# Kernel optimization log

Measured on AMD Instinct MI355X. Metric: run time of the kernel, lower is better.

Reference implementation:

```python
import jax, jax.numpy as jnp
import numpy as np

B, S, IN, E, H, NH = 32, 1024, 16, 128, 256, 4
DH = E // NH
EPS = 1e-5


def _ln(x, g, b):
    mu = jnp.mean(x, axis=-1, keepdims=True)
    var = jnp.mean(jnp.square(x - mu), axis=-1, keepdims=True)
    return (x - mu) * jax.lax.rsqrt(var + EPS) * g + b


def setup_inputs() -> dict:
    key = jax.random.key(0)
    ks = iter(jax.random.split(key, 32))
    n = lambda shape, s=0.02: jax.random.normal(next(ks), shape, jnp.float32) * s
    inp = {
        "x": jax.random.normal(next(ks), (B, S, IN), jnp.float32),
        "mask": jax.random.uniform(next(ks), (B, S), jnp.float32),
        "embed_w": n((E, IN)), "embed_b": jnp.zeros((E,), jnp.float32),
        # 3 encoder layers, params stacked on leading layer axis
        "in_proj_w": n((3, 3 * E, E)), "in_proj_b": jnp.zeros((3, 3 * E), jnp.float32),
        "out_w": n((3, E, E)), "out_b": jnp.zeros((3, E), jnp.float32),
        "ln1_g": jnp.ones((3, E), jnp.float32), "ln1_b": jnp.zeros((3, E), jnp.float32),
        "ln2_g": jnp.ones((3, E), jnp.float32), "ln2_b": jnp.zeros((3, E), jnp.float32),
        "ffn_w1": n((3, E, E)), "ffn_b1": jnp.zeros((3, E), jnp.float32),
        "ffn_w2": n((3, E, E)), "ffn_b2": jnp.zeros((3, E), jnp.float32),
        "cls_w1": n((H, E)), "cls_b1": jnp.zeros((H,), jnp.float32),
        "cls_w2": n((H, H)), "cls_b2": jnp.zeros((H,), jnp.float32),
        "cls_w3": n((H, H)), "cls_b3": jnp.zeros((H,), jnp.float32),
        "cls_w4": n((1, H)), "cls_b4": jnp.zeros((1,), jnp.float32),
    }
    return inp


def _encoder_layer(x, ipw, ipb, ow, ob, g1, b1, g2, b2, w1, fb1, w2, fb2):
    # PyTorch TransformerEncoderLayer, norm_first=False (post-norm), relu FFN
    qkv = x @ ipw.T + ipb                      # [B,S,3E]
    q, k, v = jnp.split(qkv, 3, axis=-1)
    q = q.reshape(B, S, NH, DH).transpose(0, 2, 1, 3)
    k = k.reshape(B, S, NH, DH).transpose(0, 2, 1, 3)
    v = v.reshape(B, S, NH, DH).transpose(0, 2, 1, 3)
    scores = jnp.einsum("bhqd,bhkd->bhqk", q, k) / np.sqrt(DH)  # naive O(S^2) math SDPA
    attn = jax.nn.softmax(scores, axis=-1)
    o = jnp.einsum("bhqk,bhkd->bhqd", attn, v)
    o = o.transpose(0, 2, 1, 3).reshape(B, S, E) @ ow.T + ob
    x = _ln(x + o, g1, b1)
    ff = jax.nn.relu(x @ w1.T + fb1) @ w2.T + fb2
    return _ln(x + ff, g2, b2)


def reference(x, mask, embed_w, embed_b, in_proj_w, in_proj_b, out_w, out_b,
              ln1_g, ln1_b, ln2_g, ln2_b, ffn_w1, ffn_b1, ffn_w2, ffn_b2,
              cls_w1, cls_b1, cls_w2, cls_b2, cls_w3, cls_b3, cls_w4, cls_b4):
    h = jax.nn.relu(x @ embed_w.T + embed_b)   # [B,S,E]
    for i in range(3):
        h = _encoder_layer(h, in_proj_w[i], in_proj_b[i], out_w[i], out_b[i],
                           ln1_g[i], ln1_b[i], ln2_g[i], ln2_b[i],
                           ffn_w1[i], ffn_b1[i], ffn_w2[i], ffn_b2[i])
    pooled = jnp.sum(h * mask[:, :, None], axis=1)  # [B,E] masked sum pool
    z = jax.nn.relu(pooled @ cls_w1.T + cls_b1)
    z = jax.nn.relu(z @ cls_w2.T + cls_b2)
    z = jax.nn.relu(z @ cls_w3.T + cls_b3)
    return jax.nn.sigmoid(z @ cls_w4.T + cls_b4)    # [B,1]
```

## Files before the change

### kernel.cpp

```cpp
#include <hip/hip_runtime.h>
#include <hip/hip_bf16.h>
#include <math.h>

#define B 32
#define S 1024
#define IN_DIM 16
#define E 128
#define NH 4
#define DH 32
#define HDIM 256
#define ROWS (B*S)
#define EPS 1e-5f

#define N_IPW (3*384*128)
#define N_SQ  (3*128*128)
#define NCVT ((N_IPW + 3*N_SQ) / 256)

typedef __bf16 bf16x8 __attribute__((ext_vector_type(8)));
typedef __bf16 bf16x4 __attribute__((ext_vector_type(4)));
typedef __bf16 bf16x2 __attribute__((ext_vector_type(2)));
typedef float f32x4 __attribute__((ext_vector_type(4)));

#define MFMA16 __builtin_amdgcn_mfma_f32_16x16x32_bf16

union BF2U { bf16x2 b; unsigned int u; };
__device__ inline unsigned int pk2(float a, float b) {
    BF2U x; x.b[0] = (__bf16)a; x.b[1] = (__bf16)b; return x.u;
}

union U8 { bf16x8 v8; bf16x4 v4[2]; };
__device__ inline void st8(__bf16* p, bf16x8 v) {
    U8 u; u.v8 = v;
    *(bf16x4*)p = u.v4[0];
    *(bf16x4*)(p + 4) = u.v4[1];
}
__device__ inline bf16x8 ld8(const __bf16* p) {
    U8 u;
    u.v4[0] = *(const bf16x4*)p;
    u.v4[1] = *(const bf16x4*)(p + 4);
    return u.v8;
}

__global__ __launch_bounds__(256) void k_embedcvt(
        const float* __restrict__ ipw, const float* __restrict__ ow,
        const float* __restrict__ w1, const float* __restrict__ w2,
        __bf16* __restrict__ wbo,
        const float* __restrict__ x, const float* __restrict__ W,
        const float* __restrict__ bias, __bf16* __restrict__ hb)
{
    int t = threadIdx.x;
    if (blockIdx.x < NCVT) {
        int i = blockIdx.x * 256 + t;
        float v;
        if (i < N_IPW) v = ipw[i];
        else if (i < N_IPW + N_SQ) v = ow[i - N_IPW];
        else if (i < N_IPW + 2 * N_SQ) v = w1[i - N_IPW - N_SQ];
        else v = w2[i - N_IPW - 2 * N_SQ];
        wbo[i] = (__bf16)v;
        return;
    }
    int row0 = (blockIdx.x - NCVT) * 16;
    __shared__ float xs[16][16];
    xs[t >> 4][t & 15] = x[(row0 + (t >> 4)) * IN_DIM + (t & 15)];
    __syncthreads();
    int sub = t >> 7, tc = t & 127;
    float w[16];
#pragma unroll
    for (int i = 0; i < 16; ++i) w[i] = W[tc * 16 + i];
    float bb = bias[tc];
#pragma unroll
    for (int rr = 0; rr < 8; ++rr) {
        int lr = sub * 8 + rr;
        float acc = bb;
#pragma unroll
        for (int i = 0; i < 16; ++i) acc += xs[lr][i] * w[i];
        hb[(size_t)(row0 + lr) * E + tc] = (__bf16)fmaxf(acc, 0.f);
    }
}

__global__ __launch_bounds__(1024, 4) void k_qkvattn(
        const __bf16* __restrict__ hb, const __bf16* __restrict__ Wip,
        const float* __restrict__ bip, __bf16* __restrict__ O)
{
    __shared__ __attribute__((aligned(16))) __bf16 Ksh[1024][36];
    __shared__ __attribute__((aligned(16))) __bf16 Vsh[32][1036];
    __shared__ __attribute__((aligned(16))) __bf16 Pm[16][16][36];

    int t = threadIdx.x, lane = t & 63, wv = t >> 6;
    int l15 = lane & 15, quad = lane >> 4;
    int lb = ((blockIdx.x & 7) << 5) | (blockIdx.x >> 3);
    int half = lb & 1, bh = lb >> 1;
    int hh = bh & 3, b = bh >> 2;

    const __bf16* hpanel = hb + (size_t)b * S * E;

    const float qscale = 0.1767766952966369f * 1.4426950408889634f * 8388608.0f;
    const float C2 = 1065101558.0f;
    const f32x4 cinit = {C2, C2, C2, C2};
    const f32x4 z4 = {0.f, 0.f, 0.f, 0.f};

    int qrow0 = half * 512 + wv * 32;
    bf16x8 bQ[2];
    {
        bf16x8 bWq[2][4];
#pragma unroll
        for (int df = 0; df < 2; ++df)
#pragma unroll
            for (int kc = 0; kc < 4; ++kc)
                bWq[df][kc] = *(const bf16x8*)&Wip[(size_t)(hh*32 + df*16 + l15)*128 + kc*32 + quad*8];
        float bq0 = bip[hh*32 + l15], bq1 = bip[hh*32 + 16 + l15];
#pragma unroll
        for (int qf = 0; qf < 2; ++qf) {
            bf16x8 af[4];
#pragma unroll
            for (int kc = 0; kc < 4; ++kc)
                af[kc] = *(const bf16x8*)&hpanel[(size_t)(qrow0 + qf*16 + l15)*128 + kc*32 + quad*8];
            f32x4 a0 = z4, a1 = z4;
#pragma unroll
            for (int kc = 0; kc < 4; ++kc) {
                a0 = MFMA16(af[kc], bWq[0][kc], a0, 0, 0, 0);
                a1 = MFMA16(af[kc], bWq[1][kc], a1, 0, 0, 0);
            }
#pragma unroll
            for (int r = 0; r < 4; ++r) {
                Pm[wv][quad*4 + r][l15]      = (__bf16)((a0[r] + bq0) * qscale);
                Pm[wv][quad*4 + r][16 + l15] = (__bf16)((a1[r] + bq1) * qscale);
            }
            __asm__ __volatile__("" ::: "memory");
            bQ[qf] = ld8(&Pm[wv][l15][quad*8]);
            __asm__ __volatile__("" ::: "memory");
        }
    }

    {
        bf16x8 bWk[2][4], bWv[2][4];
#pragma unroll
        for (int df = 0; df < 2; ++df)
#pragma unroll
            for (int kc = 0; kc < 4; ++kc) {
                bWk[df][kc] = *(const bf16x8*)&Wip[(size_t)(128 + hh*32 + df*16 + l15)*128 + kc*32 + quad*8];
                bWv[df][kc] = *(const bf16x8*)&Wip[(size_t)(256 + hh*32 + df*16 + l15)*128 + kc*32 + quad*8];
            }
        float bk0 = bip[128 + hh*32 + l15],  bk1 = bip[128 + hh*32 + 16 + l15];
        float bvb0 = bip[256 + hh*32 + l15], bvb1 = bip[256 + hh*32 + 16 + l15];
#pragma unroll
        for (int c = 0; c < 4; ++c) {
            int srow = c*256 + wv*16 + l15;
            bf16x8 af[4];
#pragma unroll
            for (int kc = 0; kc < 4; ++kc)
                af[kc] = *(const bf16x8*)&hpanel[(size_t)srow*128 + kc*32 + quad*8];
            f32x4 k0 = z4, k1 = z4, v0 = z4, v1 = z4;
#pragma unroll
            for (int kc = 0; kc < 4; ++kc) {
                k0 = MFMA16(af[kc], bWk[0][kc], k0, 0, 0, 0);
                k1 = MFMA16(af[kc], bWk[1][kc], k1, 0, 0, 0);
                v0 = MFMA16(af[kc], bWv[0][kc], v0, 0, 0, 0);
                v1 = MFMA16(af[kc], bWv[1][kc], v1, 0, 0, 0);
            }
            int s0 = c*256 + wv*16 + quad*4;
#pragma unroll
            for (int r = 0; r < 4; ++r) {
                Ksh[s0 + r][l15]      = (__bf16)(k0[r] + bk0);
                Ksh[s0 + r][16 + l15] = (__bf16)(k1[r] + bk1);
            }
            uint2 u0, u1;
            u0.x = pk2(v0[0] + bvb0, v0[1] + bvb0);
            u0.y = pk2(v0[2] + bvb0, v0[3] + bvb0);
            u1.x = pk2(v1[0] + bvb1, v1[1] + bvb1);
            u1.y = pk2(v1[2] + bvb1, v1[3] + bvb1);
            *(uint2*)&Vsh[l15][s0] = u0;
            *(uint2*)&Vsh[16 + l15][s0] = u1;
        }
    }
    __syncthreads();

    bf16x8 vones;
#pragma unroll
    for (int j = 0; j < 8; ++j) vones[j] = (__bf16)1.0f;
    f32x4 o[2][2], ol[2];
#pragma unroll
    for (int qf = 0; qf < 2; ++qf) {
        ol[qf] = z4; o[qf][0] = z4; o[qf][1] = z4;
    }

    for (int c = 0; c < 16; ++c) {
        bf16x8 aK[4], bV[2][2];
#pragma unroll
        for (int ck = 0; ck < 4; ++ck)
            aK[ck] = ld8(&Ksh[c*64 + ck*16 + l15][quad*8]);
#pragma unroll
        for (int kc = 0; kc < 2; ++kc) {
            bV[kc][0] = ld8(&Vsh[l15][c*64 + kc*32 + quad*8]);
            bV[kc][1] = ld8(&Vsh[16 + l15][c*64 + kc*32 + quad*8]);
        }
#pragma unroll
        for (int qf = 0; qf < 2; ++qf) {
            f32x4 sf[4];
#pragma unroll
            for (int ck = 0; ck < 4; ++ck)
                sf[ck] = MFMA16(aK[ck], bQ[qf], cinit, 0, 0, 0);
            uint2 u[4];
#pragma unroll
            for (int ck = 0; ck < 4; ++ck) {
                int i0 = (int)sf[ck][0];
                int i1 = (int)sf[ck][1];
                int i2 = (int)sf[ck][2];
                int i3 = (int)sf[ck][3];
                u[ck].x = __builtin_amdgcn_perm((unsigned)i1, (unsigned)i0, 0x07060302u);
                u[ck].y = __builtin_amdgcn_perm((unsigned)i3, (unsigned)i2, 0x07060302u);
            }
            *(uint2*)&Pm[wv][l15][quad*4]      = u[0];
            *(uint2*)&Pm[wv][l15][16 + quad*4] = u[1];
            __asm__ __volatile__("" ::: "memory");
            {
                bf16x8 ap = ld8(&Pm[wv][l15][quad*8]);
                o[qf][0] = MFMA16(ap, bV[0][0], o[qf][0], 0, 0, 0);
                o[qf][1] = MFMA16(ap, bV[0][1], o[qf][1], 0, 0, 0);
                ol[qf]   = MFMA16(ap, vones, ol[qf], 0, 0, 0);
            }
            __asm__ __volatile__("" ::: "memory");
            *(uint2*)&Pm[wv][l15][quad*4]      = u[2];
            *(uint2*)&Pm[wv][l15][16 + quad*4] = u[3];
            __asm__ __volatile__("" ::: "memory");
            {
                bf16x8 ap = ld8(&Pm[wv][l15][quad*8]);
                o[qf][0] = MFMA16(ap, bV[1][0], o[qf][0], 0, 0, 0);
                o[qf][1] = MFMA16(ap, bV[1][1], o[qf][1], 0, 0, 0);
                ol[qf]   = MFMA16(ap, vones, ol[qf], 0, 0, 0);
            }
            __asm__ __volatile__("" ::: "memory");
        }
    }

#pragma unroll
    for (int qf = 0; qf < 2; ++qf)
#pragma unroll
        for (int r = 0; r < 4; ++r) {
            float linv = 1.f / ol[qf][r];
            int row = half*512 + wv*32 + qf*16 + quad*4 + r;
            __bf16* op = O + ((size_t)(b * S) + row) * E + hh*32;
            op[l15]      = (__bf16)(o[qf][0][r] * linv);
            op[16 + l15] = (__bf16)(o[qf][1][r] * linv);
        }
}

__global__ __launch_bounds__(512, 4) void k_layer2(const __bf16* __restrict__ t0b,
        const __bf16* __restrict__ Wo, const float* __restrict__ ob,
        const float* __restrict__ g1, const float* __restrict__ bt1,
        const __bf16* __restrict__ W1, const float* __restrict__ b1v,
        const __bf16* __restrict__ W2, const float* __restrict__ b2v,
        const float* __restrict__ g2, const float* __restrict__ bt2,
        __bf16* __restrict__ hb)
{
    __shared__ __attribute__((aligned(16))) __bf16 As[64][132];
    __shared__ __attribute__((aligned(16))) __bf16 Ws[128][132];
    __shared__ float red[2][64][2];
    int t = threadIdx.x;
    int m0 = blockIdx.x * 64;
    int arow = t >> 3, acol = (t & 7) * 16;
    int wrow = t >> 2, wcol = (t & 3) * 32;
    {
        const __bf16* Ap = t0b + (size_t)(m0 + arow) * 128 + acol;
#pragma unroll
        for (int j = 0; j < 2; ++j)
            st8(&As[arow][acol + j * 8], *(const bf16x8*)&Ap[j * 8]);
        const __bf16* Wp = Wo + (size_t)wrow * 128 + wcol;
#pragma unroll
        for (int j = 0; j < 4; ++j)
            st8(&Ws[wrow][wcol + j * 8], *(const bf16x8*)&Wp[j * 8]);
    }
    __syncthreads();
    int lane = t & 63, wv = t >> 6;
    int l15 = lane & 15, quad = lane >> 4;
    int nh = wv & 1, mh = wv >> 1;
    f32x4 acc[4];

#pragma unroll
    for (int i = 0; i < 4; ++i) acc[i] = (f32x4){0.f, 0.f, 0.f, 0.f};
#pragma unroll
    for (int kc = 0; kc < 4; ++kc) {
        bf16x8 aw[4], ba;
#pragma unroll
        for (int nc = 0; nc < 4; ++nc)
            aw[nc] = ld8(&Ws[nh * 64 + nc * 16 + l15][kc * 32 + quad * 8]);
        ba = ld8(&As[mh * 16 + l15][kc * 32 + quad * 8]);
#pragma unroll
        for (int nc = 0; nc < 4; ++nc)
            acc[nc] = MFMA16(aw[nc], ba, acc[nc], 0, 0, 0);
    }
    float s1 = 0.f, s2 = 0.f;
    int m = m0 + mh * 16 + l15;
#pragma unroll
    for (int nc = 0; nc < 4; ++nc) {
        float4 bv = *(const float4*)&ob[nh * 64 + nc * 16 + quad * 4];
        bf16x4 rv = *(const bf16x4*)&hb[(size_t)m * 128 + nh * 64 + nc * 16 + quad * 4];
        acc[nc][0] += bv.x + (float)rv[0];
        acc[nc][1] += bv.y + (float)rv[1];
        acc[nc][2] += bv.z + (float)rv[2];
        acc[nc][3] += bv.w + (float)rv[3];
#pragma unroll
        for (int i = 0; i < 4; ++i) {
            s1 += acc[nc][i];
            s2 += acc[nc][i] * acc[nc][i];
        }
    }
    s1 += __shfl_xor(s1, 16); s1 += __shfl_xor(s1, 32);
    s2 += __shfl_xor(s2, 16); s2 += __shfl_xor(s2, 32);
    if (quad == 0) {
        red[nh][mh * 16 + l15][0] = s1;
        red[nh][mh * 16 + l15][1] = s2;
    }
    __syncthreads();
    float mu, rs;
    {
        int r = mh * 16 + l15;
        float S1 = red[0][r][0] + red[1][r][0];
        float S2 = red[0][r][1] + red[1][r][1];
        mu = S1 * (1.f / 128.f);
        float var = S2 * (1.f / 128.f) - mu * mu;
        rs = rsqrtf(var + EPS);
    }
    bf16x4 res2[4];
#pragma unroll
    for (int nc = 0; nc < 4; ++nc) {
        float4 gv = *(const float4*)&g1[nh * 64 + nc * 16 + quad * 4];
        float4 bb = *(const float4*)&bt1[nh * 64 + nc * 16 + quad * 4];
        float o0 = (acc[nc][0] - mu) * rs * gv.x + bb.x;
        float o1 = (acc[nc][1] - mu) * rs * gv.y + bb.y;
        float o2 = (acc[nc][2] - mu) * rs * gv.z + bb.z;
        float o3 = (acc[nc][3] - mu) * rs * gv.w + bb.w;
        bf16x4 xb;
        xb[0] = (__bf16)o0; xb[1] = (__bf16)o1;
        xb[2] = (__bf16)o2; xb[3] = (__bf16)o3;
        res2[nc] = xb;
        *(bf16x4*)&As[mh * 16 + l15][nh * 64 + nc * 16 + quad * 4] = xb;
    }
    {
        const __bf16* Wp = W1 + (size_t)wrow * 128 + wcol;
#pragma unroll
        for (int j = 0; j < 4; ++j)
            st8(&Ws[wrow][wcol + j * 8], *(const bf16x8*)&Wp[j * 8]);
    }
    __syncthreads();

#pragma unroll
    for (int i = 0; i < 4; ++i) acc[i] = (f32x4){0.f, 0.f, 0.f, 0.f};
#pragma unroll
    for (int kc = 0; kc < 4; ++kc) {
        bf16x8 aw[4], ba;
#pragma unroll
        for (int nc = 0; nc < 4; ++nc)
            aw[nc] = ld8(&Ws[nh * 64 + nc * 16 + l15][kc * 32 + quad * 8]);
        ba = ld8(&As[mh * 16 + l15][kc * 32 + quad * 8]);
#pragma unroll
        for (int nc = 0; nc < 4; ++nc)
            acc[nc] = MFMA16(aw[nc], ba, acc[nc], 0, 0, 0);
    }
    __syncthreads();
#pragma unroll
    for (int nc = 0; nc < 4; ++nc) {
        float4 bv = *(const float4*)&b1v[nh * 64 + nc * 16 + quad * 4];
        float v0 = fmaxf(acc[nc][0] + bv.x, 0.f);
        float v1 = fmaxf(acc[nc][1] + bv.y, 0.f);
        float v2 = fmaxf(acc[nc][2] + bv.z, 0.f);
        float v3 = fmaxf(acc[nc][3] + bv.w, 0.f);
        uint2 u; u.x = pk2(v0, v1); u.y = pk2(v2, v3);
        *(uint2*)&As[mh * 16 + l15][nh * 64 + nc * 16 + quad * 4] = u;
    }
    {
        const __bf16* Wp = W2 + (size_t)wrow * 128 + wcol;
#pragma unroll
        for (int j = 0; j < 4; ++j)
            st8(&Ws[wrow][wcol + j * 8], *(const bf16x8*)&Wp[j * 8]);
    }
    __syncthreads();

#pragma unroll
    for (int i = 0; i < 4; ++i) acc[i] = (f32x4){0.f, 0.f, 0.f, 0.f};
#pragma unroll
    for (int kc = 0; kc < 4; ++kc) {
        bf16x8 aw[4], ba;
#pragma unroll
        for (int nc = 0; nc < 4; ++nc)
            aw[nc] = ld8(&Ws[nh * 64 + nc * 16 + l15][kc * 32 + quad * 8]);
        ba = ld8(&As[mh * 16 + l15][kc * 32 + quad * 8]);
#pragma unroll
        for (int nc = 0; nc < 4; ++nc)
            acc[nc] = MFMA16(aw[nc], ba, acc[nc], 0, 0, 0);
    }
    s1 = 0.f; s2 = 0.f;
#pragma unroll
    for (int nc = 0; nc < 4; ++nc) {
        float4 bv = *(const float4*)&b2v[nh * 64 + nc * 16 + quad * 4];
        acc[nc][0] += bv.x + (float)res2[nc][0];
        acc[nc][1] += bv.y + (float)res2[nc][1];
        acc[nc][2] += bv.z + (float)res2[nc][2];
        acc[nc][3] += bv.w + (float)res2[nc][3];
#pragma unroll
        for (int i = 0; i < 4; ++i) {
            s1 += acc[nc][i];
            s2 += acc[nc][i] * acc[nc][i];
        }
    }
    s1 += __shfl_xor(s1, 16); s1 += __shfl_xor(s1, 32);
    s2 += __shfl_xor(s2, 16); s2 += __shfl_xor(s2, 32);
    if (quad == 0) {
        red[nh][mh * 16 + l15][0] = s1;
        red[nh][mh * 16 + l15][1] = s2;
    }
    __syncthreads();
    {
        int r = mh * 16 + l15;
        float S1 = red[0][r][0] + red[1][r][0];
        float S2 = red[0][r][1] + red[1][r][1];
        mu = S1 * (1.f / 128.f);
        float var = S2 * (1.f / 128.f) - mu * mu;
        rs = rsqrtf(var + EPS);
    }
#pragma unroll
    for (int nc = 0; nc < 4; ++nc) {
        float4 gv = *(const float4*)&g2[nh * 64 + nc * 16 + quad * 4];
        float4 bb = *(const float4*)&bt2[nh * 64 + nc * 16 + quad * 4];
        float o0 = (acc[nc][0] - mu) * rs * gv.x + bb.x;
        float o1 = (acc[nc][1] - mu) * rs * gv.y + bb.y;
        float o2 = (acc[nc][2] - mu) * rs * gv.z + bb.z;
        float o3 = (acc[nc][3] - mu) * rs * gv.w + bb.w;
        uint2 u; u.x = pk2(o0, o1); u.y = pk2(o2, o3);
        *(uint2*)&hb[(size_t)m * 128 + nh * 64 + nc * 16 + quad * 4] = u;
    }
}

__global__ __launch_bounds__(128) void k_pool1(const __bf16* __restrict__ h,
        const float* __restrict__ mask, float* __restrict__ part)
{
    int bx = blockIdx.x;
    int b = bx >> 3, ch = bx & 7, t = threadIdx.x;
    float acc = 0.f;
    const __bf16* hp = h + (size_t)(b * S + ch * 128) * E + t;
    const float* mp = mask + b * S + ch * 128;
    for (int s = 0; s < 128; ++s) acc += (float)hp[(size_t)s * E] * mp[s];
    part[(size_t)bx * E + t] = acc;
}

__global__ __launch_bounds__(256) void k_head(const float* __restrict__ part,
        const float* __restrict__ cw1, const float* __restrict__ cb1,
        const float* __restrict__ cw2, const float* __restrict__ cb2,
        const float* __restrict__ cw3, const float* __restrict__ cb3,
        const float* __restrict__ cw4, const float* __restrict__ cb4,
        float* __restrict__ out)
{
    int b = blockIdx.x, t = threadIdx.x;
    __shared__ float p[128], za[256], zb[256];
    __shared__ float red4[4];
    if (t < 128) {
        float a = 0.f;
#pragma unroll
        for (int c = 0; c < 8; ++c) a += part[(size_t)(b * 8 + c) * 128 + t];
        p[t] = a;
    }
    __syncthreads();
    float a1 = cb1[t];
    for (int k = 0; k < 128; ++k) a1 += p[k] * cw1[t * 128 + k];
    za[t] = fmaxf(a1, 0.f);
    __syncthreads();
    float a2 = cb2[t];
    for (int k = 0; k < 256; ++k) a2 += za[k] * cw2[t * 256 + k];
    zb[t] = fmaxf(a2, 0.f);
    __syncthreads();
    float a3 = cb3[t];
    for (int k = 0; k < 256; ++k) a3 += zb[k] * cw3[t * 256 + k];
    float z3 = fmaxf(a3, 0.f);
    float prt = z3 * cw4[t];
#pragma unroll
    for (int o2 = 32; o2; o2 >>= 1) prt += __shfl_xor(prt, o2);
    if ((t & 63) == 0) red4[t >> 6] = prt;
    __syncthreads();
    if (t == 0) {
        float sum = red4[0] + red4[1] + red4[2] + red4[3] + cb4[0];
        out[b] = 1.f / (1.f + __expf(-sum));
    }
}

extern "C" void kernel_launch(void* const* d_in, const int* in_sizes, int n_in,
                              void* d_out, int out_size, void* d_ws, size_t ws_size,
                              hipStream_t stream)
{
    const float* x     = (const float*)d_in[0];
    const float* mask  = (const float*)d_in[1];
    const float* emb_w = (const float*)d_in[2];
    const float* emb_b = (const float*)d_in[3];
    const float* ipw   = (const float*)d_in[4];
    const float* ipb   = (const float*)d_in[5];
    const float* ow    = (const float*)d_in[6];
    const float* ob    = (const float*)d_in[7];
    const float* ln1g  = (const float*)d_in[8];
    const float* ln1b  = (const float*)d_in[9];
    const float* ln2g  = (const float*)d_in[10];
    const float* ln2b  = (const float*)d_in[11];
    const float* w1    = (const float*)d_in[12];
    const float* fb1   = (const float*)d_in[13];
    const float* w2    = (const float*)d_in[14];
    const float* fb2   = (const float*)d_in[15];
    const float* cw1   = (const float*)d_in[16];
    const float* cb1   = (const float*)d_in[17];
    const float* cw2   = (const float*)d_in[18];
    const float* cb2   = (const float*)d_in[19];
    const float* cw3   = (const float*)d_in[20];
    const float* cb3   = (const float*)d_in[21];
    const float* cw4   = (const float*)d_in[22];
    const float* cb4   = (const float*)d_in[23];

    char* p = (char*)d_ws;
    __bf16* hb   = (__bf16*)p;   p += (size_t)ROWS * E * 2;
    p += (size_t)ROWS * 256 * 2;
    p += (size_t)ROWS * 32 * 4 * 2 / 4;
    __bf16* t0b  = (__bf16*)p;   p += (size_t)ROWS * E * 2;
    __bf16* wb   = (__bf16*)p;   p += (size_t)(N_IPW + 3 * N_SQ) * 2;
    float* part  = (float*)p;    p += (size_t)B * 8 * E * 4;

    __bf16* wb_ipw = wb;
    __bf16* wb_ow  = wb + N_IPW;
    __bf16* wb_w1  = wb_ow + N_SQ;
    __bf16* wb_w2  = wb_w1 + N_SQ;

    k_embedcvt<<<NCVT + ROWS / 16, 256, 0, stream>>>(
        ipw, ow, w1, w2, wb, x, emb_w, emb_b, hb);
    for (int L = 0; L < 3; ++L) {
        k_qkvattn<<<B * NH * 2, 1024, 0, stream>>>(
            hb, wb_ipw + (size_t)L * 384 * 128, ipb + L * 384, t0b);
        k_layer2<<<ROWS / 64, 512, 0, stream>>>(
            t0b, wb_ow + (size_t)L * 128 * 128, ob + L * 128,
            ln1g + L * E, ln1b + L * E,
            wb_w1 + (size_t)L * 128 * 128, fb1 + L * 128,
            wb_w2 + (size_t)L * 128 * 128, fb2 + L * 128,
            ln2g + L * E, ln2b + L * E, hb);
    }
    k_pool1<<<B * 8, 128, 0, stream>>>(hb, mask, part);
    k_head<<<B, 256, 0, stream>>>(part, cw1, cb1, cw2, cb2, cw3, cb3, cw4, cb4,
                                  (float*)d_out);
}
```

Before: 316.5 us.

## Switch attention kernel to 32x32 MFMA tiles with register-resident probabilities

Rewrites the attention inner loop to use 32x32x16 bf16 MFMA instead of 16x16x32, with each wave owning 64 query rows. The S tile's accumulator layout is packed straight into the A operand for the PV MFMA, so the LDS round-trip through Pm is no longer needed. The block drops to 512 threads, and the K/V projection loop gains software prefetch of the next h tile. The larger tiles are meant to cut LDS traffic and MFMA issue count, at the cost of more registers per wave and fewer waves per block.

Measured after the change: 291.7 us. 7.8% less time.

```diff
diff --git a/kernel.cpp b/kernel.cpp
--- a/kernel.cpp
+++ b/kernel.cpp
@@ -20,15 +20,17 @@
 typedef __bf16 bf16x4 __attribute__((ext_vector_type(4)));
 typedef __bf16 bf16x2 __attribute__((ext_vector_type(2)));
 typedef float f32x4 __attribute__((ext_vector_type(4)));
+typedef float f32x16 __attribute__((ext_vector_type(16)));
 
 #define MFMA16 __builtin_amdgcn_mfma_f32_16x16x32_bf16
+#define MFMA32 __builtin_amdgcn_mfma_f32_32x32x16_bf16
 
 union BF2U { bf16x2 b; unsigned int u; };
 __device__ inline unsigned int pk2(float a, float b) {
     BF2U x; x.b[0] = (__bf16)a; x.b[1] = (__bf16)b; return x.u;
 }
 
-union U8 { bf16x8 v8; bf16x4 v4[2]; };
+union U8 { bf16x8 v8; bf16x4 v4[2]; unsigned u4[4]; };
 __device__ inline void st8(__bf16* p, bf16x8 v) {
     U8 u; u.v8 = v;
     *(bf16x4*)p = u.v4[0];
@@ -78,16 +80,17 @@
     }
 }
 
-__global__ __launch_bounds__(1024, 4) void k_qkvattn(
+__global__ __launch_bounds__(512, 2) void k_qkvattn(
         const __bf16* __restrict__ hb, const __bf16* __restrict__ Wip,
         const float* __restrict__ bip, __bf16* __restrict__ O)
 {
     __shared__ __attribute__((aligned(16))) __bf16 Ksh[1024][36];
     __shared__ __attribute__((aligned(16))) __bf16 Vsh[32][1036];
-    __shared__ __attribute__((aligned(16))) __bf16 Pm[16][16][36];
+    __shared__ __attribute__((aligned(16))) __bf16 Pm[8][32][36];
 
     int t = threadIdx.x, lane = t & 63, wv = t >> 6;
     int l15 = lane & 15, quad = lane >> 4;
+    int l31 = lane & 31, hi = lane >> 5;
     int lb = ((blockIdx.x & 7) << 5) | (blockIdx.x >> 3);
     int half = lb & 1, bh = lb >> 1;
     int hh = bh & 3, b = bh >> 2;
@@ -96,38 +99,34 @@
 
     const float qscale = 0.1767766952966369f * 1.4426950408889634f * 8388608.0f;
     const float C2 = 1065101558.0f;
-    const f32x4 cinit = {C2, C2, C2, C2};
-    const f32x4 z4 = {0.f, 0.f, 0.f, 0.f};
-
-    int qrow0 = half * 512 + wv * 32;
-    bf16x8 bQ[2];
-    {
-        bf16x8 bWq[2][4];
-#pragma unroll
-        for (int df = 0; df < 2; ++df)
-#pragma unroll
-            for (int kc = 0; kc < 4; ++kc)
-                bWq[df][kc] = *(const bf16x8*)&Wip[(size_t)(hh*32 + df*16 + l15)*128 + kc*32 + quad*8];
-        float bq0 = bip[hh*32 + l15], bq1 = bip[hh*32 + 16 + l15];
-#pragma unroll
-        for (int qf = 0; qf < 2; ++qf) {
-            bf16x8 af[4];
-#pragma unroll
-            for (int kc = 0; kc < 4; ++kc)
-                af[kc] = *(const bf16x8*)&hpanel[(size_t)(qrow0 + qf*16 + l15)*128 + kc*32 + quad*8];
-            f32x4 a0 = z4, a1 = z4;
-#pragma unroll
-            for (int kc = 0; kc < 4; ++kc) {
-                a0 = MFMA16(af[kc], bWq[0][kc], a0, 0, 0, 0);
-                a1 = MFMA16(af[kc], bWq[1][kc], a1, 0, 0, 0);
-            }
-#pragma unroll
-            for (int r = 0; r < 4; ++r) {
-                Pm[wv][quad*4 + r][l15]      = (__bf16)((a0[r] + bq0) * qscale);
-                Pm[wv][quad*4 + r][16 + l15] = (__bf16)((a1[r] + bq1) * qscale);
+    f32x16 cinit16, z16;
+#pragma unroll
+    for (int i = 0; i < 16; ++i) { cinit16[i] = C2; z16[i] = 0.f; }
+
+    bf16x8 bQ[2][2];
+    {
+        bf16x8 bWq[8];
+#pragma unroll
+        for (int ch = 0; ch < 8; ++ch)
+            bWq[ch] = *(const bf16x8*)&Wip[(size_t)(hh*32 + l31)*128 + ch*16 + hi*8];
+        float bq = bip[hh*32 + l31];
+#pragma unroll
+        for (int qt = 0; qt < 2; ++qt) {
+            int qrow0 = half*512 + wv*64 + qt*32;
+            f32x16 aq = z16;
+#pragma unroll
+            for (int ch = 0; ch < 8; ++ch) {
+                bf16x8 ah = *(const bf16x8*)&hpanel[(size_t)(qrow0 + l31)*128 + ch*16 + hi*8];
+                aq = MFMA32(ah, bWq[ch], aq, 0, 0, 0);
+            }
+#pragma unroll
+            for (int r = 0; r < 16; ++r) {
+                int q = (r & 3) + 8*(r >> 2) + 4*hi;
+                Pm[wv][q][l31] = (__bf16)((aq[r] + bq) * qscale);
             }
             __asm__ __volatile__("" ::: "memory");
-            bQ[qf] = ld8(&Pm[wv][l15][quad*8]);
+            bQ[qt][0] = ld8(&Pm[wv][l31][hi*8]);
+            bQ[qt][1] = ld8(&Pm[wv][l31][16 + hi*8]);
             __asm__ __volatile__("" ::: "memory");
         }
     }
@@ -143,13 +142,18 @@
             }
         float bk0 = bip[128 + hh*32 + l15],  bk1 = bip[128 + hh*32 + 16 + l15];
         float bvb0 = bip[256 + hh*32 + l15], bvb1 = bip[256 + hh*32 + 16 + l15];
-#pragma unroll
-        for (int c = 0; c < 4; ++c) {
-            int srow = c*256 + wv*16 + l15;
-            bf16x8 af[4];
-#pragma unroll
-            for (int kc = 0; kc < 4; ++kc)
-                af[kc] = *(const bf16x8*)&hpanel[(size_t)srow*128 + kc*32 + quad*8];
+        int srow = wv*16 + l15;
+        bf16x8 af[4], ag[4];
+#pragma unroll
+        for (int kc = 0; kc < 4; ++kc)
+            af[kc] = *(const bf16x8*)&hpanel[(size_t)srow*128 + kc*32 + quad*8];
+        const f32x4 z4 = {0.f, 0.f, 0.f, 0.f};
+        for (int c = 0; c < 8; ++c) {
+            if (c < 7) {
+#pragma unroll
+                for (int kc = 0; kc < 4; ++kc)
+                    ag[kc] = *(const bf16x8*)&hpanel[(size_t)((c+1)*128 + srow)*128 + kc*32 + quad*8];
+            }
             f32x4 k0 = z4, k1 = z4, v0 = z4, v1 = z4;
 #pragma unroll
             for (int kc = 0; kc < 4; ++kc) {
@@ -158,7 +162,7 @@
                 v0 = MFMA16(af[kc], bWv[0][kc], v0, 0, 0, 0);
                 v1 = MFMA16(af[kc], bWv[1][kc], v1, 0, 0, 0);
             }
-            int s0 = c*256 + wv*16 + quad*4;
+            int s0 = c*128 + wv*16 + quad*4;
 #pragma unroll
             for (int r = 0; r < 4; ++r) {
                 Ksh[s0 + r][l15]      = (__bf16)(k0[r] + bk0);
@@ -171,6 +175,8 @@
             u1.y = pk2(v1[2] + bvb1, v1[3] + bvb1);
             *(uint2*)&Vsh[l15][s0] = u0;
             *(uint2*)&Vsh[16 + l15][s0] = u1;
+#pragma unroll
+            for (int kc = 0; kc < 4; ++kc) af[kc] = ag[kc];
         }
     }
     __syncthreads();
@@ -178,70 +184,58 @@
     bf16x8 vones;
 #pragma unroll
     for (int j = 0; j < 8; ++j) vones[j] = (__bf16)1.0f;
-    f32x4 o[2][2], ol[2];
-#pragma unroll
-    for (int qf = 0; qf < 2; ++qf) {
-        ol[qf] = z4; o[qf][0] = z4; o[qf][1] = z4;
-    }
+    f32x16 o[2], ol[2];
+    o[0] = z16; o[1] = z16; ol[0] = z16; ol[1] = z16;
 
     for (int c = 0; c < 16; ++c) {
-        bf16x8 aK[4], bV[2][2];
-#pragma unroll
-        for (int ck = 0; ck < 4; ++ck)
-            aK[ck] = ld8(&Ksh[c*64 + ck*16 + l15][quad*8]);
-#pragma unroll
-        for (int kc = 0; kc < 2; ++kc) {
-            bV[kc][0] = ld8(&Vsh[l15][c*64 + kc*32 + quad*8]);
-            bV[kc][1] = ld8(&Vsh[16 + l15][c*64 + kc*32 + quad*8]);
-        }
-#pragma unroll
-        for (int qf = 0; qf < 2; ++qf) {
-            f32x4 sf[4];
-#pragma unroll
-            for (int ck = 0; ck < 4; ++ck)
-                sf[ck] = MFMA16(aK[ck], bQ[qf], cinit, 0, 0, 0);
-            uint2 u[4];
-#pragma unroll
-            for (int ck = 0; ck < 4; ++ck) {
-                int i0 = (int)sf[ck][0];
-                int i1 = (int)sf[ck][1];
-                int i2 = (int)sf[ck][2];
-                int i3 = (int)sf[ck][3];
-                u[ck].x = __builtin_amdgcn_perm((unsigned)i1, (unsigned)i0, 0x07060302u);
-                u[ck].y = __builtin_amdgcn_perm((unsigned)i3, (unsigned)i2, 0x07060302u);
-            }
-            *(uint2*)&Pm[wv][l15][quad*4]      = u[0];
-            *(uint2*)&Pm[wv][l15][16 + quad*4] = u[1];
-            __asm__ __volatile__("" ::: "memory");
-            {
-                bf16x8 ap = ld8(&Pm[wv][l15][quad*8]);
-                o[qf][0] = MFMA16(ap, bV[0][0], o[qf][0], 0, 0, 0);
-                o[qf][1] = MFMA16(ap, bV[0][1], o[qf][1], 0, 0, 0);
-                ol[qf]   = MFMA16(ap, vones, ol[qf], 0, 0, 0);
-            }
-            __asm__ __volatile__("" ::: "memory");
-            *(uint2*)&Pm[wv][l15][quad*4]      = u[2];
-            *(uint2*)&Pm[wv][l15][16 + quad*4] = u[3];
-            __asm__ __volatile__("" ::: "memory");
-            {
-                bf16x8 ap = ld8(&Pm[wv][l15][quad*8]);
-                o[qf][0] = MFMA16(ap, bV[1][0], o[qf][0], 0, 0, 0);
-                o[qf][1] = MFMA16(ap, bV[1][1], o[qf][1], 0, 0, 0);
-                ol[qf]   = MFMA16(ap, vones, ol[qf], 0, 0, 0);
-            }
-            __asm__ __volatile__("" ::: "memory");
-        }
-    }
-
-#pragma unroll
-    for (int qf = 0; qf < 2; ++qf)
-#pragma unroll
-        for (int r = 0; r < 4; ++r) {
-            float linv = 1.f / ol[qf][r];
-            int row = half*512 + wv*32 + qf*16 + quad*4 + r;
-            __bf16* op = O + ((size_t)(b * S) + row) * E + hh*32;
-            op[l15]      = (__bf16)(o[qf][0][r] * linv);
-            op[16 + l15] = (__bf16)(o[qf][1][r] * linv);
+        bf16x8 aK[2][2];
+#pragma unroll
+        for (int sub = 0; sub < 2; ++sub)
+#pragma unroll
+            for (int dh = 0; dh < 2; ++dh)
+                aK[sub][dh] = ld8(&Ksh[c*64 + sub*32 + l31][dh*16 + hi*8]);
+        bf16x8 bVf[4];
+#pragma unroll
+        for (int ch = 0; ch < 4; ++ch) {
+            U8 u;
+            const __bf16* vp = &Vsh[l31][c*64 + ch*16 + hi*4];
+            u.v4[0] = *(const bf16x4*)vp;
+            u.v4[1] = *(const bf16x4*)(vp + 8);
+            bVf[ch] = u.v8;
+        }
+#pragma unroll
+        for (int qt = 0; qt < 2; ++qt) {
+#pragma unroll
+            for (int sub = 0; sub < 2; ++sub) {
+                f32x16 acc = cinit16;
+                acc = MFMA32(aK[sub][0], bQ[qt][0], acc, 0, 0, 0);
+                acc = MFMA32(aK[sub][1], bQ[qt][1], acc, 0, 0, 0);
+#pragma unroll
+                for (int g = 0; g < 2; ++g) {
+                    U8 u;
+#pragma unroll
+                    for (int r = 0; r < 4; ++r) {
+                        int ia = (int)acc[g*8 + 2*r];
+                        int ib = (int)acc[g*8 + 2*r + 1];
+                        u.u4[r] = __builtin_amdgcn_perm((unsigned)ib, (unsigned)ia, 0x07060302u);
+                    }
+                    bf16x8 ap = u.v8;
+                    int ch = sub*2 + g;
+                    o[qt]  = MFMA32(ap, bVf[ch], o[qt], 0, 0, 0);
+                    ol[qt] = MFMA32(ap, vones,  ol[qt], 0, 0, 0);
+                }
+            }
+        }
+    }
+
+#pragma unroll
+    for (int qt = 0; qt < 2; ++qt)
+#pragma unroll
+        for (int r = 0; r < 16; ++r) {
+            float linv = 1.f / ol[qt][r];
+            int q = (r & 3) + 8*(r >> 2) + 4*hi;
+            int row = half*512 + wv*64 + qt*32 + q;
+            O[((size_t)(b * S) + row) * E + hh*32 + l31] = (__bf16)(o[qt][r] * linv);
         }
 }
 
@@ -527,7 +521,7 @@
     k_embedcvt<<<NCVT + ROWS / 16, 256, 0, stream>>>(
         ipw, ow, w1, w2, wb, x, emb_w, emb_b, hb);
     for (int L = 0; L < 3; ++L) {
-        k_qkvattn<<<B * NH * 2, 1024, 0, stream>>>(
+        k_qkvattn<<<B * NH * 2, 512, 0, stream>>>(
             hb, wb_ipw + (size_t)L * 384 * 128, ipb + L * 384, t0b);
         k_layer2<<<ROWS / 64, 512, 0, stream>>>(
             t0b, wb_ow + (size_t)L * 128 * 128, ob + L * 128,
```
